# Optimization experiments

Hardware: AMD Instinct MI355X
Metric: run time of the kernel (lower is better)

The kernel has to match this reference:

```python
import jax, jax.numpy as jnp
import numpy as np

B, NQ, NK = 16, 1024, 1024
DQ = DK = DV = 512
H = 4
DH = DV // H  # 128


def layer_norm(x, g, b, eps=1e-5):
    mu = jnp.mean(x, axis=-1, keepdims=True)
    var = jnp.var(x, axis=-1, keepdims=True)  # biased, matches torch LayerNorm
    return (x - mu) / jnp.sqrt(var + eps) * g + b


def setup_inputs() -> dict:
    key = jax.random.key(0)
    ks = jax.random.split(key, 16)
    s = lambda d: 1.0 / np.sqrt(d)
    return {
        "Q": jax.random.normal(ks[0], (B, NQ, DQ), jnp.float32),
        "K": jax.random.normal(ks[1], (B, NK, DK), jnp.float32),
        "weights": jax.random.uniform(ks[2], (H * B, NQ, NK), jnp.float32),
        "Wq": jax.random.normal(ks[3], (DV, DQ), jnp.float32) * s(DQ),
        "bq": jnp.zeros((DV,), jnp.float32),
        "Wk": jax.random.normal(ks[4], (DV, DK), jnp.float32) * s(DK),
        "bk": jnp.zeros((DV,), jnp.float32),
        "Wv": jax.random.normal(ks[5], (DV, DK), jnp.float32) * s(DK),
        "bv": jnp.zeros((DV,), jnp.float32),
        "Wo": jax.random.normal(ks[6], (DV, DV), jnp.float32) * s(DV),
        "bo": jnp.zeros((DV,), jnp.float32),
        "g0": jnp.ones((DV,), jnp.float32),
        "beta0": jnp.zeros((DV,), jnp.float32),
        "g1": jnp.ones((DV,), jnp.float32),
        "beta1": jnp.zeros((DV,), jnp.float32),
    }


def reference(Q, K, weights, Wq, bq, Wk, bk, Wv, bv, Wo, bo, g0, beta0, g1, beta1):
    q = Q @ Wq.T + bq  # [B,NQ,DV]
    k = K @ Wk.T + bk  # [B,NK,DV]
    v = K @ Wv.T + bv  # [B,NK,DV]

    # torch split(dh, 2) + cat(0) == head-major [H,B,N,DH]
    def heads(x, n):
        return x.reshape(B, n, H, DH).transpose(2, 0, 1, 3)

    q_, k_, v_ = heads(q, NQ), heads(k, NK), heads(v, NK)

    # NOTE: original scales by sqrt(dim_V), not sqrt(head_dim)
    scores = jnp.einsum("hbqd,hbkd->hbqk", q_, k_) / np.sqrt(DV)
    log_w = jnp.log(jnp.clip(weights, 0.0, None)).reshape(H, B, NQ, NK)
    A = jax.nn.softmax(scores + log_w, axis=-1)  # [H,B,NQ,NK]

    o = q_ + jnp.einsum("hbqk,hbkd->hbqd", A, v_)  # residual inside heads
    # split(B,0)+cat(2) == merge heads back to [B,NQ,DV]
    O = o.transpose(1, 2, 0, 3).reshape(B, NQ, DV)
    O = layer_norm(O, g0, beta0)
    O = O + jax.nn.relu(O @ Wo.T + bo)
    O = layer_norm(O, g1, beta1)
    return O
```

## Files before the change

kernel.cpp:

```cpp
#include <hip/hip_runtime.h>

typedef unsigned short u16;
typedef unsigned int u32;
typedef __attribute__((ext_vector_type(8))) short short8;
typedef __attribute__((ext_vector_type(4))) float f32x4;
typedef __attribute__((ext_vector_type(2))) u32 uintx2;
typedef __attribute__((address_space(3))) u32 lds32;
typedef const __attribute__((address_space(1))) u32 g32c;

__device__ __forceinline__ u16 f2bf(float f) {
  union { float f; u32 u; } v; v.f = f;
  return (u16)((v.u + 0x7fffu + ((v.u >> 16) & 1u)) >> 16);
}
__device__ __forceinline__ float bf2f(u16 h) {
  union { u32 u; float f; } v; v.u = ((u32)h) << 16;
  return v.f;
}

__global__ void cvt_w_kernel(const float* __restrict__ Wq, const float* __restrict__ Wk,
                             const float* __restrict__ Wv, const float* __restrict__ Wo,
                             u16* __restrict__ dst) {
  int m = blockIdx.y;
  const float* s = (m == 0) ? Wq : (m == 1) ? Wk : (m == 2) ? Wv : Wo;
  int idx = (blockIdx.x * 256 + threadIdx.x) * 4;
  float4 v = *(const float4*)(s + idx);
  uintx2 pk;
  pk[0] = (u32)f2bf(v.x) | ((u32)f2bf(v.y) << 16);
  pk[1] = (u32)f2bf(v.z) | ((u32)f2bf(v.w) << 16);
  *(uintx2*)(dst + m * 262144 + idx) = pk;
}

template <bool AF32, bool OUTMODE>
__device__ __forceinline__ void gemm_bt_body(const void* __restrict__ Ap,
                                             const u16* __restrict__ Bw,
                                             const float* __restrict__ bias,
                                             u16* __restrict__ C) {
  __shared__ u16 ldsA[128 * 64];
  __shared__ u16 ldsB[128 * 64];
  const int t = threadIdx.x;
  const int lane = t & 63, wid = t >> 6;
  const int lr = lane & 15, lg = lane >> 4;
  const int n0 = blockIdx.x * 128;
  const int m0 = blockIdx.y * 128;
  const int wr = (wid >> 1) * 64, wc = (wid & 1) * 64;

  f32x4 acc[4][4];
#pragma unroll
  for (int i = 0; i < 4; ++i)
#pragma unroll
    for (int j = 0; j < 4; ++j)
#pragma unroll
      for (int r = 0; r < 4; ++r) acc[i][j][r] = 0.f;

  for (int kt = 0; kt < 512; kt += 64) {
    __syncthreads();
#pragma unroll
    for (int i = 0; i < 4; ++i) {
      int lin = i * 256 + t;
      int row = lin >> 3, u = lin & 7;
      int pu = u ^ (row & 7);
      if constexpr (AF32) {
        const float* src = (const float*)Ap + (size_t)(m0 + row) * 512 + kt + u * 8;
        float4 v0 = *(const float4*)src;
        float4 v1 = *(const float4*)(src + 4);
        short8 pk;
        pk[0] = (short)f2bf(v0.x); pk[1] = (short)f2bf(v0.y);
        pk[2] = (short)f2bf(v0.z); pk[3] = (short)f2bf(v0.w);
        pk[4] = (short)f2bf(v1.x); pk[5] = (short)f2bf(v1.y);
        pk[6] = (short)f2bf(v1.z); pk[7] = (short)f2bf(v1.w);
        *(short8*)&ldsA[row * 64 + pu * 8] = pk;
      } else {
        const u16* src = (const u16*)Ap + (size_t)(m0 + row) * 512 + kt + u * 8;
        *(short8*)&ldsA[row * 64 + pu * 8] = *(const short8*)src;
      }
      const u16* bsrc = Bw + (size_t)(n0 + row) * 512 + kt + u * 8;
      *(short8*)&ldsB[row * 64 + pu * 8] = *(const short8*)bsrc;
    }
    __syncthreads();
#pragma unroll
    for (int kk = 0; kk < 2; ++kk) {
      short8 af[4], bfr[4];
#pragma unroll
      for (int mf = 0; mf < 4; ++mf) {
        int row = wr + mf * 16 + lr;
        af[mf] = *(const short8*)&ldsA[row * 64 + (((kk * 4 + lg) ^ (row & 7)) * 8)];
      }
#pragma unroll
      for (int nf = 0; nf < 4; ++nf) {
        int row = wc + nf * 16 + lr;
        bfr[nf] = *(const short8*)&ldsB[row * 64 + (((kk * 4 + lg) ^ (row & 7)) * 8)];
      }
#pragma unroll
      for (int mf = 0; mf < 4; ++mf)
#pragma unroll
        for (int nf = 0; nf < 4; ++nf)
          acc[mf][nf] =
              __builtin_amdgcn_mfma_f32_16x16x32_bf16(af[mf], bfr[nf], acc[mf][nf], 0, 0, 0);
    }
  }

#pragma unroll
  for (int mf = 0; mf < 4; ++mf)
#pragma unroll
    for (int nf = 0; nf < 4; ++nf) {
      int c = n0 + wc + nf * 16 + lr;
      float bv = bias[c];
#pragma unroll
      for (int r = 0; r < 4; ++r) {
        int rr = m0 + wr + mf * 16 + lg * 4 + r;
        float v = acc[mf][nf][r] + bv;
        if constexpr (OUTMODE) {
          v = v > 0.f ? v : 0.f;
          v += bf2f(((const u16*)Ap)[(size_t)rr * 512 + c]);
        }
        C[(size_t)rr * 512 + c] = f2bf(v);
      }
    }
}

__global__ __launch_bounds__(256) void gemm3_kernel(const float* __restrict__ Q,
                                                    const float* __restrict__ K,
                                                    const u16* __restrict__ Wb,
                                                    const float* __restrict__ bq,
                                                    const float* __restrict__ bk,
                                                    const float* __restrict__ bv,
                                                    u16* qb, u16* kb, u16* vb) {
  int z = blockIdx.z;
  const void* Ap = (z == 0) ? (const void*)Q : (const void*)K;
  const u16* Bw = Wb + z * 262144;
  const float* bias = (z == 0) ? bq : (z == 1) ? bk : bv;
  u16* C = (z == 0) ? qb : (z == 1) ? kb : vb;
  gemm_bt_body<true, false>(Ap, Bw, bias, C);
}

__global__ __launch_bounds__(256) void gemmo_kernel(const u16* __restrict__ X,
                                                    const u16* __restrict__ Wb,
                                                    const float* __restrict__ bo,
                                                    u16* Z) {
  gemm_bt_body<false, true>(X, Wb, bo, Z);
}

__global__ __launch_bounds__(256) void attn_kernel(const u16* __restrict__ qb,
                                                   const u16* __restrict__ kb,
                                                   const u16* __restrict__ vb,
                                                   const float* __restrict__ Wt,
                                                   u16* __restrict__ Ob) {
  __shared__ __align__(16) u16 ldsK[2][64 * 128];
  __shared__ __align__(16) u16 ldsV[2][64 * 128];
  __shared__ __align__(16) u16 ldsP[128 * 64];
  const int t = threadIdx.x;
  const int lane = t & 63, wid = t >> 6;
  const int lr = lane & 15, lg = lane >> 4;
  const int hb = blockIdx.y;
  const int b = hb & 15;
  const int h = hb >> 4;
  const int q0 = blockIdx.x * 128;
  const int wq = wid * 32;
  const size_t kvbase = ((size_t)b * 1024) * 512 + h * 128;
  const float SCALE = 0.044194173824159216f;

  const u16* ksrc[4];
#pragma unroll
  for (int i = 0; i < 4; ++i) {
    int lin = i * 256 + t;
    int row = lin >> 4, u = lin & 15;
    ksrc[i] = kb + kvbase + (size_t)row * 512 + ((u ^ (row & 15)) * 8);
  }
  const ptrdiff_t dkv = vb - kb;
  const int wslot = (t & 192) * 8;

#define STAGE(bu)                                                                          \
  do {                                                                                     \
    _Pragma("unroll") for (int i_ = 0; i_ < 4; ++i_) {                                     \
      __builtin_amdgcn_global_load_lds((g32c*)(ksrc[i_]),                                  \
                                       (lds32*)(&ldsK[bu][i_ * 2048 + wslot]), 16, 0, 0);  \
      __builtin_amdgcn_global_load_lds((g32c*)(ksrc[i_] + dkv),                            \
                                       (lds32*)(&ldsV[bu][i_ * 2048 + wslot]), 16, 0, 0);  \
      ksrc[i_] += 32768;                                           \
    }                                                                                      \
  } while (0)

  const float* wp0 = Wt + ((size_t)hb * 1024 + q0 + wq + lr) * 1024 + lg * 4;
  const float* wp1 = wp0 + 16 * 1024;

#define WLOADP(W)                                          \
  do {                                                     \
    _Pragma("unroll") for (int j_ = 0; j_ < 4; ++j_) {     \
      W[j_]     = *(const f32x4*)(wp0 + j_ * 16);          \
      W[4 + j_] = *(const f32x4*)(wp1 + j_ * 16);          \
    }                                                      \
    wp0 += 64; wp1 += 64;                                  \
  } while (0)

  short8 qfr[2][4];
#pragma unroll
  for (int nf = 0; nf < 2; ++nf) {
    const u16* qp = qb + kvbase + (size_t)(q0 + wq + nf * 16 + lr) * 512 + lg * 8;
#pragma unroll
    for (int ds = 0; ds < 4; ++ds) qfr[nf][ds] = *(const short8*)(qp + ds * 32);
  }

  f32x4 oacc[2][8];
#pragma unroll
  for (int i = 0; i < 2; ++i)
#pragma unroll
    for (int j = 0; j < 8; ++j)
#pragma unroll
      for (int r = 0; r < 4; ++r) oacc[i][j][r] = 0.f;
  float lacc[2] = {0.f, 0.f};

  auto tile_compute = [&](const u16* bK, const u16* bV, const f32x4 (&W)[8]) {
    f32x4 sacc[4][2];
#pragma unroll
    for (int i = 0; i < 4; ++i)
#pragma unroll
      for (int j = 0; j < 2; ++j)
#pragma unroll
        for (int r = 0; r < 4; ++r) sacc[i][j][r] = 0.f;

#pragma unroll
    for (int ds = 0; ds < 4; ++ds) {
      short8 kf[4];
#pragma unroll
      for (int mf = 0; mf < 4; ++mf) {
        int row = mf * 16 + lr;
        kf[mf] = *(const short8*)&bK[row * 128 + (((ds * 4 + lg) ^ (row & 15)) * 8)];
      }
#pragma unroll
      for (int mf = 0; mf < 4; ++mf)
#pragma unroll
        for (int nf = 0; nf < 2; ++nf)
          sacc[mf][nf] =
              __builtin_amdgcn_mfma_f32_16x16x32_bf16(kf[mf], qfr[nf][ds], sacc[mf][nf], 0, 0, 0);
    }

#pragma unroll
    for (int nf = 0; nf < 2; ++nf) {
      int prow = wq + nf * 16 + lr;
#pragma unroll
      for (int mf = 0; mf < 4; ++mf) {
        f32x4 w4 = W[nf * 4 + mf];
        float p0 = w4[0] * __expf(sacc[mf][nf][0] * SCALE);
        float p1 = w4[1] * __expf(sacc[mf][nf][1] * SCALE);
        float p2 = w4[2] * __expf(sacc[mf][nf][2] * SCALE);
        float p3 = w4[3] * __expf(sacc[mf][nf][3] * SCALE);
        lacc[nf] += (p0 + p1) + (p2 + p3);
        uintx2 pk;
        pk[0] = (u32)f2bf(p0) | ((u32)f2bf(p1) << 16);
        pk[1] = (u32)f2bf(p2) | ((u32)f2bf(p3) << 16);
        int byteoff = (prow * 128 + (mf * 16 + lg * 4) * 2) ^ ((prow & 7) << 4);
        *(uintx2*)((char*)ldsP + byteoff) = pk;
      }
    }

#pragma unroll
    for (int ks = 0; ks < 2; ++ks) {
      short8 pa[2];
#pragma unroll
      for (int qf = 0; qf < 2; ++qf) {
        int row = wq + qf * 16 + lr;
        int byteoff = (row * 128 + (ks * 4 + lg) * 16) ^ ((row & 7) << 4);
        pa[qf] = *(const short8*)((const char*)ldsP + byteoff);
      }
      short8 vf[8];
#pragma unroll
      for (int nf = 0; nf < 8; ++nf) {
        int ch = nf * 2 + (lr >> 3);
        int cl = lr & 7;
        u32 pk[4];
#pragma unroll
        for (int jp = 0; jp < 4; ++jp) {
          int k0 = ks * 32 + lg * 8 + jp * 2;
          int k1 = k0 + 1;
          u32 a = bV[k0 * 128 + ((ch ^ (k0 & 15)) * 8) + cl];
          u32 c2 = bV[k1 * 128 + ((ch ^ (k1 & 15)) * 8) + cl];
          pk[jp] = a | (c2 << 16);
        }
        union { u32 u[4]; short8 s; } fu;
        fu.u[0] = pk[0]; fu.u[1] = pk[1]; fu.u[2] = pk[2]; fu.u[3] = pk[3];
        vf[nf] = fu.s;
      }
#pragma unroll
      for (int qf = 0; qf < 2; ++qf)
#pragma unroll
        for (int nf = 0; nf < 8; ++nf)
          oacc[qf][nf] =
              __builtin_amdgcn_mfma_f32_16x16x32_bf16(pa[qf], vf[nf], oacc[qf][nf], 0, 0, 0);
    }
  };

#define SCHED_FENCE() __builtin_amdgcn_sched_barrier(0)
#define WAITBAR(N)                                                 \
  do {                                                             \
    SCHED_FENCE();                                                 \
    asm volatile("s_waitcnt vmcnt(" #N ")" ::: "memory");          \
    __builtin_amdgcn_s_barrier();                                  \
    SCHED_FENCE();                                                 \
  } while (0)
#define BAR()                                                      \
  do {                                                             \
    SCHED_FENCE();                                                 \
    __builtin_amdgcn_s_barrier();                                  \
    SCHED_FENCE();                                                 \
  } while (0)

  STAGE(0);

  for (int it = 0; it < 8; ++it) {
    {
      f32x4 w[8];
      WLOADP(w);
      STAGE(1);
      WAITBAR(16);
      tile_compute(&ldsK[0][0], &ldsV[0][0], w);
      BAR();
    }
    {
      f32x4 w[8];
      WLOADP(w);
      if (it < 7) {
        STAGE(0);
        WAITBAR(16);
      } else {
        WAITBAR(8);
      }
      tile_compute(&ldsK[1][0], &ldsV[1][0], w);
      if (it < 7) BAR();
    }
  }

  float lred[2];
#pragma unroll
  for (int nf = 0; nf < 2; ++nf) {
    float s = lacc[nf];
    s += __shfl_xor(s, 16);
    s += __shfl_xor(s, 32);
    lred[nf] = s;
  }

#pragma unroll
  for (int qf = 0; qf < 2; ++qf)
#pragma unroll
    for (int r = 0; r < 4; ++r) {
      float lv = __shfl(lred[qf], (lane & 48) | (lg * 4 + r));
      float linv = 1.0f / lv;
      int qrow = q0 + wq + qf * 16 + lg * 4 + r;
      size_t base = kvbase + (size_t)qrow * 512;
#pragma unroll
      for (int nf = 0; nf < 8; ++nf) {
        size_t idx = base + nf * 16 + lr;
        Ob[idx] = f2bf(bf2f(qb[idx]) + oacc[qf][nf][r] * linv);
      }
    }
#undef STAGE
#undef WLOADP
#undef WAITBAR
#undef BAR
#undef SCHED_FENCE
}

template <bool F32OUT>
__global__ __launch_bounds__(256) void ln_kernel(const u16* __restrict__ in,
                                                 const float* __restrict__ g,
                                                 const float* __restrict__ be,
                                                 void* __restrict__ outp) {
  const int lane = threadIdx.x & 63, wid = threadIdx.x >> 6;
  const int row = blockIdx.x * 4 + wid;
  const u16* p = in + (size_t)row * 512 + lane * 8;
  short8 v = *(const short8*)p;
  float x[8];
  float s = 0.f, s2 = 0.f;
#pragma unroll
  for (int j = 0; j < 8; ++j) {
    x[j] = bf2f((u16)v[j]);
    s += x[j];
    s2 += x[j] * x[j];
  }
#pragma unroll
  for (int off = 1; off < 64; off <<= 1) {
    s += __shfl_xor(s, off);
    s2 += __shfl_xor(s2, off);
  }
  float mu = s * (1.f / 512.f);
  float var = s2 * (1.f / 512.f) - mu * mu;
  float rs = rsqrtf(var + 1e-5f);
  float4 ga = *(const float4*)(g + lane * 8);
  float4 gb = *(const float4*)(g + lane * 8 + 4);
  float4 ba = *(const float4*)(be + lane * 8);
  float4 bb = *(const float4*)(be + lane * 8 + 4);
  float gg[8] = {ga.x, ga.y, ga.z, ga.w, gb.x, gb.y, gb.z, gb.w};
  float bv[8] = {ba.x, ba.y, ba.z, ba.w, bb.x, bb.y, bb.z, bb.w};
  if constexpr (F32OUT) {
    float* out = (float*)outp + (size_t)row * 512 + lane * 8;
    float4 o0, o1;
    o0.x = (x[0] - mu) * rs * gg[0] + bv[0];
    o0.y = (x[1] - mu) * rs * gg[1] + bv[1];
    o0.z = (x[2] - mu) * rs * gg[2] + bv[2];
    o0.w = (x[3] - mu) * rs * gg[3] + bv[3];
    o1.x = (x[4] - mu) * rs * gg[4] + bv[4];
    o1.y = (x[5] - mu) * rs * gg[5] + bv[5];
    o1.z = (x[6] - mu) * rs * gg[6] + bv[6];
    o1.w = (x[7] - mu) * rs * gg[7] + bv[7];
    *(float4*)out = o0;
    *(float4*)(out + 4) = o1;
  } else {
    short8 o;
#pragma unroll
    for (int j = 0; j < 8; ++j) o[j] = (short)f2bf((x[j] - mu) * rs * gg[j] + bv[j]);
    *(short8*)((u16*)outp + (size_t)row * 512 + lane * 8) = o;
  }
}

extern "C" void kernel_launch(void* const* d_in, const int* in_sizes, int n_in,
                              void* d_out, int out_size, void* d_ws, size_t ws_size,
                              hipStream_t stream) {
  (void)in_sizes; (void)n_in; (void)out_size; (void)ws_size;
  const float* Q   = (const float*)d_in[0];
  const float* K   = (const float*)d_in[1];
  const float* Wt  = (const float*)d_in[2];
  const float* Wq  = (const float*)d_in[3];
  const float* bq  = (const float*)d_in[4];
  const float* Wk  = (const float*)d_in[5];
  const float* bk  = (const float*)d_in[6];
  const float* Wv  = (const float*)d_in[7];
  const float* bv  = (const float*)d_in[8];
  const float* Wo  = (const float*)d_in[9];
  const float* bo  = (const float*)d_in[10];
  const float* g0  = (const float*)d_in[11];
  const float* be0 = (const float*)d_in[12];
  const float* g1  = (const float*)d_in[13];
  const float* be1 = (const float*)d_in[14];

  char* ws = (char*)d_ws;
  const size_t MB16 = 16777216;
  u16* qb = (u16*)(ws);
  u16* kb = (u16*)(ws + MB16);
  u16* vb = (u16*)(ws + 2 * MB16);
  u16* Wb = (u16*)(ws + 3 * MB16);
  u16* Ob = (u16*)d_out;

  cvt_w_kernel<<<dim3(256, 4), 256, 0, stream>>>(Wq, Wk, Wv, Wo, Wb);
  gemm3_kernel<<<dim3(4, 128, 3), 256, 0, stream>>>(Q, K, Wb, bq, bk, bv, qb, kb, vb);
  attn_kernel<<<dim3(8, 64), 256, 0, stream>>>(qb, kb, vb, Wt, Ob);
  ln_kernel<false><<<4096, 256, 0, stream>>>(Ob, g0, be0, qb);
  gemmo_kernel<<<dim3(4, 128), 256, 0, stream>>>(qb, Wb + 786432, bo, kb);
  ln_kernel<true><<<4096, 256, 0, stream>>>(kb, g1, be1, d_out);
}
```

Baseline: 277.9 us.

## Store V transposed per head from projection GEMM and prefetch weight tiles earlier

The V projection epilogue now writes V in a head-major transposed layout [B,H,DH,NK], so the attention kernel can load V fragments for the PV MFMA with single 16-byte LDS reads instead of gathering 16-bit elements and packing them. Staging of V tiles into LDS is changed to match the new layout. In addition, the weights-tile loads are double-buffered across iterations so the next tile's global loads are issued before the current compute. This costs extra registers for the second weight buffer, and the transposed epilogue writes are narrower and strided.

```diff
diff --git a/kernel.cpp b/kernel.cpp
--- a/kernel.cpp
+++ b/kernel.cpp
@@ -30,7 +30,7 @@
   *(uintx2*)(dst + m * 262144 + idx) = pk;
 }
 
-template <bool AF32, bool OUTMODE>
+template <bool AF32, bool OUTMODE, bool TRANSV>
 __device__ __forceinline__ void gemm_bt_body(const void* __restrict__ Ap,
                                              const u16* __restrict__ Bw,
                                              const float* __restrict__ bias,
@@ -99,23 +99,41 @@
     }
   }
 
-#pragma unroll
-  for (int mf = 0; mf < 4; ++mf)
-#pragma unroll
-    for (int nf = 0; nf < 4; ++nf) {
-      int c = n0 + wc + nf * 16 + lr;
-      float bv = bias[c];
-#pragma unroll
-      for (int r = 0; r < 4; ++r) {
-        int rr = m0 + wr + mf * 16 + lg * 4 + r;
-        float v = acc[mf][nf][r] + bv;
-        if constexpr (OUTMODE) {
-          v = v > 0.f ? v : 0.f;
-          v += bf2f(((const u16*)Ap)[(size_t)rr * 512 + c]);
+  if constexpr (TRANSV) {
+    const int h_ = n0 >> 7;
+#pragma unroll
+    for (int mf = 0; mf < 4; ++mf)
+#pragma unroll
+      for (int nf = 0; nf < 4; ++nf) {
+        int d = wc + nf * 16 + lr;
+        int rr0 = m0 + wr + mf * 16 + lg * 4;
+        int b_ = rr0 >> 10;
+        int k0 = rr0 & 1023;
+        float bvv = bias[n0 + d];
+        uintx2 pk;
+        pk[0] = (u32)f2bf(acc[mf][nf][0] + bvv) | ((u32)f2bf(acc[mf][nf][1] + bvv) << 16);
+        pk[1] = (u32)f2bf(acc[mf][nf][2] + bvv) | ((u32)f2bf(acc[mf][nf][3] + bvv) << 16);
+        *(uintx2*)(C + (((size_t)b_ * 4 + h_) * 128 + d) * 1024 + k0) = pk;
+      }
+  } else {
+#pragma unroll
+    for (int mf = 0; mf < 4; ++mf)
+#pragma unroll
+      for (int nf = 0; nf < 4; ++nf) {
+        int c = n0 + wc + nf * 16 + lr;
+        float bv = bias[c];
+#pragma unroll
+        for (int r = 0; r < 4; ++r) {
+          int rr = m0 + wr + mf * 16 + lg * 4 + r;
+          float v = acc[mf][nf][r] + bv;
+          if constexpr (OUTMODE) {
+            v = v > 0.f ? v : 0.f;
+            v += bf2f(((const u16*)Ap)[(size_t)rr * 512 + c]);
+          }
+          C[(size_t)rr * 512 + c] = f2bf(v);
         }
-        C[(size_t)rr * 512 + c] = f2bf(v);
-      }
-    }
+      }
+  }
 }
 
 __global__ __launch_bounds__(256) void gemm3_kernel(const float* __restrict__ Q,
@@ -124,29 +142,33 @@
                                                     const float* __restrict__ bq,
                                                     const float* __restrict__ bk,
                                                     const float* __restrict__ bv,
-                                                    u16* qb, u16* kb, u16* vb) {
+                                                    u16* qb, u16* kb, u16* vbT) {
   int z = blockIdx.z;
-  const void* Ap = (z == 0) ? (const void*)Q : (const void*)K;
-  const u16* Bw = Wb + z * 262144;
-  const float* bias = (z == 0) ? bq : (z == 1) ? bk : bv;
-  u16* C = (z == 0) ? qb : (z == 1) ? kb : vb;
-  gemm_bt_body<true, false>(Ap, Bw, bias, C);
+  if (z == 2) {
+    gemm_bt_body<true, false, true>(K, Wb + 524288, bv, vbT);
+  } else {
+    const void* Ap = (z == 0) ? (const void*)Q : (const void*)K;
+    const u16* Bw = Wb + z * 262144;
+    const float* bias = (z == 0) ? bq : bk;
+    u16* C = (z == 0) ? qb : kb;
+    gemm_bt_body<true, false, false>(Ap, Bw, bias, C);
+  }
 }
 
 __global__ __launch_bounds__(256) void gemmo_kernel(const u16* __restrict__ X,
                                                     const u16* __restrict__ Wb,
                                                     const float* __restrict__ bo,
                                                     u16* Z) {
-  gemm_bt_body<false, true>(X, Wb, bo, Z);
+  gemm_bt_body<false, true, false>(X, Wb, bo, Z);
 }
 
 __global__ __launch_bounds__(256) void attn_kernel(const u16* __restrict__ qb,
                                                    const u16* __restrict__ kb,
-                                                   const u16* __restrict__ vb,
+                                                   const u16* __restrict__ vbT,
                                                    const float* __restrict__ Wt,
                                                    u16* __restrict__ Ob) {
   __shared__ __align__(16) u16 ldsK[2][64 * 128];
-  __shared__ __align__(16) u16 ldsV[2][64 * 128];
+  __shared__ __align__(16) u16 ldsVT[2][128 * 64];
   __shared__ __align__(16) u16 ldsP[128 * 64];
   const int t = threadIdx.x;
   const int lane = t & 63, wid = t >> 6;
@@ -157,27 +179,36 @@
   const int q0 = blockIdx.x * 128;
   const int wq = wid * 32;
   const size_t kvbase = ((size_t)b * 1024) * 512 + h * 128;
+  const size_t vtbase = ((size_t)b * 4 + h) * 131072;
   const float SCALE = 0.044194173824159216f;
 
   const u16* ksrc[4];
+  const u16* vtsrc[4];
 #pragma unroll
   for (int i = 0; i < 4; ++i) {
-    int lin = i * 256 + t;
-    int row = lin >> 4, u = lin & 15;
-    ksrc[i] = kb + kvbase + (size_t)row * 512 + ((u ^ (row & 15)) * 8);
-  }
-  const ptrdiff_t dkv = vb - kb;
+    {
+      int lin = i * 256 + t;
+      int row = lin >> 4, u = lin & 15;
+      ksrc[i] = kb + kvbase + (size_t)row * 512 + ((u ^ (row & 15)) * 8);
+    }
+    {
+      int lin = i * 256 + t;
+      int row = lin >> 3, u = lin & 7;
+      vtsrc[i] = vbT + vtbase + (size_t)row * 1024 + ((u ^ (row & 7)) * 8);
+    }
+  }
   const int wslot = (t & 192) * 8;
 
-#define STAGE(bu)                                                                          \
-  do {                                                                                     \
-    _Pragma("unroll") for (int i_ = 0; i_ < 4; ++i_) {                                     \
-      __builtin_amdgcn_global_load_lds((g32c*)(ksrc[i_]),                                  \
-                                       (lds32*)(&ldsK[bu][i_ * 2048 + wslot]), 16, 0, 0);  \
-      __builtin_amdgcn_global_load_lds((g32c*)(ksrc[i_] + dkv),                            \
-                                       (lds32*)(&ldsV[bu][i_ * 2048 + wslot]), 16, 0, 0);  \
-      ksrc[i_] += 32768;                                           \
-    }                                                                                      \
+#define STAGE(bu)                                                                           \
+  do {                                                                                      \
+    _Pragma("unroll") for (int i_ = 0; i_ < 4; ++i_) {                                      \
+      __builtin_amdgcn_global_load_lds((g32c*)(ksrc[i_]),                                   \
+                                       (lds32*)(&ldsK[bu][i_ * 2048 + wslot]), 16, 0, 0);   \
+      __builtin_amdgcn_global_load_lds((g32c*)(vtsrc[i_]),                                  \
+                                       (lds32*)(&ldsVT[bu][i_ * 2048 + wslot]), 16, 0, 0);  \
+      ksrc[i_] += 32768;                                                \
+      vtsrc[i_] += 64;                                                  \
+    }                                                                                       \
   } while (0)
 
   const float* wp0 = Wt + ((size_t)hb * 1024 + q0 + wq + lr) * 1024 + lg * 4;
@@ -209,7 +240,7 @@
       for (int r = 0; r < 4; ++r) oacc[i][j][r] = 0.f;
   float lacc[2] = {0.f, 0.f};
 
-  auto tile_compute = [&](const u16* bK, const u16* bV, const f32x4 (&W)[8]) {
+  auto tile_compute = [&](const u16* bK, const u16* bVT, const f32x4 (&W)[8]) {
     f32x4 sacc[4][2];
 #pragma unroll
     for (int i = 0; i < 4; ++i)
@@ -265,20 +296,8 @@
       short8 vf[8];
 #pragma unroll
       for (int nf = 0; nf < 8; ++nf) {
-        int ch = nf * 2 + (lr >> 3);
-        int cl = lr & 7;
-        u32 pk[4];
-#pragma unroll
-        for (int jp = 0; jp < 4; ++jp) {
-          int k0 = ks * 32 + lg * 8 + jp * 2;
-          int k1 = k0 + 1;
-          u32 a = bV[k0 * 128 + ((ch ^ (k0 & 15)) * 8) + cl];
-          u32 c2 = bV[k1 * 128 + ((ch ^ (k1 & 15)) * 8) + cl];
-          pk[jp] = a | (c2 << 16);
-        }
-        union { u32 u[4]; short8 s; } fu;
-        fu.u[0] = pk[0]; fu.u[1] = pk[1]; fu.u[2] = pk[2]; fu.u[3] = pk[3];
-        vf[nf] = fu.s;
+        int row = nf * 16 + lr;
+        vf[nf] = *(const short8*)&bVT[row * 64 + (((ks * 4 + lg) ^ (row & 7)) * 8)];
       }
 #pragma unroll
       for (int qf = 0; qf < 2; ++qf)
@@ -304,27 +323,27 @@
     SCHED_FENCE();                                                 \
   } while (0)
 
+  f32x4 wA[8], wB[8];
+  WLOADP(wA);
   STAGE(0);
 
   for (int it = 0; it < 8; ++it) {
     {
-      f32x4 w[8];
-      WLOADP(w);
       STAGE(1);
+      WLOADP(wB);
       WAITBAR(16);
-      tile_compute(&ldsK[0][0], &ldsV[0][0], w);
+      tile_compute(&ldsK[0][0], &ldsVT[0][0], wA);
       BAR();
     }
     {
-      f32x4 w[8];
-      WLOADP(w);
       if (it < 7) {
         STAGE(0);
+        WLOADP(wA);
         WAITBAR(16);
       } else {
-        WAITBAR(8);
-      }
-      tile_compute(&ldsK[1][0], &ldsV[1][0], w);
+        WAITBAR(0);
+      }
+      tile_compute(&ldsK[1][0], &ldsVT[1][0], wB);
       if (it < 7) BAR();
     }
   }
@@ -433,15 +452,15 @@
 
   char* ws = (char*)d_ws;
   const size_t MB16 = 16777216;
-  u16* qb = (u16*)(ws);
-  u16* kb = (u16*)(ws + MB16);
-  u16* vb = (u16*)(ws + 2 * MB16);
-  u16* Wb = (u16*)(ws + 3 * MB16);
-  u16* Ob = (u16*)d_out;
+  u16* qb  = (u16*)(ws);
+  u16* kb  = (u16*)(ws + MB16);
+  u16* vbT = (u16*)(ws + 2 * MB16);
+  u16* Wb  = (u16*)(ws + 3 * MB16);
+  u16* Ob  = (u16*)d_out;
 
   cvt_w_kernel<<<dim3(256, 4), 256, 0, stream>>>(Wq, Wk, Wv, Wo, Wb);
-  gemm3_kernel<<<dim3(4, 128, 3), 256, 0, stream>>>(Q, K, Wb, bq, bk, bv, qb, kb, vb);
-  attn_kernel<<<dim3(8, 64), 256, 0, stream>>>(qb, kb, vb, Wt, Ob);
+  gemm3_kernel<<<dim3(4, 128, 3), 256, 0, stream>>>(Q, K, Wb, bq, bk, bv, qb, kb, vbT);
+  attn_kernel<<<dim3(8, 64), 256, 0, stream>>>(qb, kb, vbT, Wt, Ob);
   ln_kernel<false><<<4096, 256, 0, stream>>>(Ob, g0, be0, qb);
   gemmo_kernel<<<dim3(4, 128), 256, 0, stream>>>(qb, Wb + 786432, bo, kb);
   ln_kernel<true><<<4096, 256, 0, stream>>>(kb, g1, be1, d_out);
```

Result: faster. 249.8 us, median of 3 (-10.1%).
